# Performance work log

Measured on AMD Instinct MI355X. Metric: run time of the kernel, lower is better.

Reference implementation:

```python
import jax, jax.numpy as jnp
import numpy as np
from jax import lax

H = 32  # hidden_dim

def _lstm_layer(x_tbd, W_ih, W_hh, b_ih, b_hh):
    """x_tbd: [T, B, D]. Returns all hidden states [T, B, H]. PyTorch gate order i,f,g,o."""
    T, B, _ = x_tbd.shape
    # Precompute input contribution for all timesteps (one big GEMM)
    xW = jnp.einsum('tbd,gd->tbg', x_tbd, W_ih) + (b_ih + b_hh)  # [T, B, 4H]
    W_hh_T = W_hh.T  # [H, 4H]

    def step(carry, xw):
        h, c = carry
        gates = xw + h @ W_hh_T  # [B, 4H]
        i, f, g, o = jnp.split(gates, 4, axis=-1)
        i = jax.nn.sigmoid(i)
        f = jax.nn.sigmoid(f)
        g = jnp.tanh(g)
        o = jax.nn.sigmoid(o)
        c = f * c + i * g
        h = o * jnp.tanh(c)
        return (h, c), h

    h0 = jnp.zeros((B, H), x_tbd.dtype)
    (_, _), hs = lax.scan(step, (h0, h0), xW)
    return hs  # [T, B, H]


def setup_inputs() -> dict:
    key = jax.random.key(0)
    ks = jax.random.split(key, 12)
    s = 0.1  # keep gates out of saturation
    return {
        'x': jax.random.normal(ks[0], (4096, 512, 4), jnp.float32),
        'W_ih0': jax.random.normal(ks[1], (4 * H, 4), jnp.float32) * s,
        'W_hh0': jax.random.normal(ks[2], (4 * H, H), jnp.float32) * s,
        'b_ih0': jax.random.normal(ks[3], (4 * H,), jnp.float32) * s,
        'b_hh0': jax.random.normal(ks[4], (4 * H,), jnp.float32) * s,
        'W_ih1': jax.random.normal(ks[5], (4 * H, H), jnp.float32) * s,
        'W_hh1': jax.random.normal(ks[6], (4 * H, H), jnp.float32) * s,
        'b_ih1': jax.random.normal(ks[7], (4 * H,), jnp.float32) * s,
        'b_hh1': jax.random.normal(ks[8], (4 * H,), jnp.float32) * s,
        'W_out': jax.random.normal(ks[9], (1, H), jnp.float32) * s,
        'b_out': jax.random.normal(ks[10], (1,), jnp.float32) * s,
    }


def reference(x, W_ih0, W_hh0, b_ih0, b_hh0, W_ih1, W_hh1, b_ih1, b_hh1, W_out, b_out):
    # x: [B, T, D] (batch_first). Eval mode -> inter-layer dropout is identity.
    x_tbd = jnp.transpose(x, (1, 0, 2))  # [T, B, D]
    h1 = _lstm_layer(x_tbd, W_ih0, W_hh0, b_ih0, b_hh0)  # [T, B, H]
    h2 = _lstm_layer(h1, W_ih1, W_hh1, b_ih1, b_hh1)     # [T, B, H]
    last = h2[-1]  # [B, H] == out[:, -1, :]
    return last @ W_out.T + b_out  # [B, 1]
```

## Files before the change

### kernel.cpp

```cpp
#include <hip/hip_runtime.h>
#include <cmath>

constexpr int T   = 512;
constexpr int D   = 4;
constexpr int H   = 32;
constexpr int BT  = 16;
constexpr int BLK = 256;

constexpr float LOG2E     = 1.44269504088896340736f;
constexpr float NEG2LOG2E = -2.88539008177792681472f;

constexpr int XSTRIDE = 4104;
constexpr int HSTR = 40;

typedef short bf8 __attribute__((ext_vector_type(8)));
typedef float f4  __attribute__((ext_vector_type(4)));
typedef float f2  __attribute__((ext_vector_type(2)));

static __device__ __forceinline__ short bf16_rtn(float v) {
    unsigned u = __float_as_uint(v);
    u += 0x7FFFu + ((u >> 16) & 1u);
    return (short)(u >> 16);
}

__global__ __launch_bounds__(BLK, 1) void lstm_bf16p(
    const float* __restrict__ x,
    const float* __restrict__ W_ih0, const float* __restrict__ W_hh0,
    const float* __restrict__ b_ih0, const float* __restrict__ b_hh0,
    const float* __restrict__ W_ih1, const float* __restrict__ W_hh1,
    const float* __restrict__ b_ih1, const float* __restrict__ b_hh1,
    const float* __restrict__ W_out, const float* __restrict__ b_out,
    float* __restrict__ out)
{
    __shared__ __align__(16) short xbf[16 * XSTRIDE];
    __shared__ __align__(16) short h0b[2][16][HSTR];
    __shared__ __align__(16) short h1b[2][16][HSTR];
    __shared__ __align__(16) float h1f[16][36];

    const int tid   = threadIdx.x;
    const int w     = tid >> 6;
    const int lane  = tid & 63;
    const int q     = lane >> 4;
    const int nl    = lane & 15;
    const int layer = w >> 1;
    const int ug    = (w & 1) << 4;
    const int b0    = blockIdx.x * BT;

    for (int idx = tid; idx < 16 * T; idx += BLK) {
        const int col = idx & 15;
        const int t   = idx >> 4;
        float4 xv = *(const float4*)(x + ((size_t)(b0 + col) * T + t) * D);
        bf8 v = {0, 0, 0, 0, 0, 0, 0, 0};
        v[0] = bf16_rtn(xv.x); v[1] = bf16_rtn(xv.y);
        v[2] = bf16_rtn(xv.z); v[3] = bf16_rtn(xv.w);
        *(bf8*)&xbf[col * XSTRIDE + t * 8] = v;
    }
    for (int idx = tid; idx < 2 * 16 * HSTR; idx += BLK) {
        (&h0b[0][0][0])[idx] = 0;
        (&h1b[0][0][0])[idx] = 0;
    }

    const float* W1 = layer ? W_ih1 : W_hh0;
    bf8 w1[4], w2[4];
    f4  bias[4];
    #pragma unroll
    for (int g = 0; g < 4; ++g) {
        const float sc = (g == 2) ? NEG2LOG2E : -LOG2E;
        const int row = 32 * g + ug + nl;
        #pragma unroll
        for (int j = 0; j < 8; ++j) {
            w1[g][j] = bf16_rtn(W1[row * H + 8 * q + j] * sc);
            float v2 = layer ? W_hh1[row * H + 8 * q + j]
                             : ((q == 0 && j < 4) ? W_ih0[row * D + j] : 0.0f);
            w2[g][j] = bf16_rtn(v2 * sc);
        }
        #pragma unroll
        for (int r = 0; r < 4; ++r) {
            const int gr = 32 * g + ug + 4 * q + r;
            bias[g][r] = sc * (layer ? (b_ih1[gr] + b_hh1[gr])
                                     : (b_ih0[gr] + b_hh0[gr]));
        }
    }

    f2 cA; cA.x = 0.0f; cA.y = 0.0f;
    f2 cB; cB.x = 0.0f; cB.y = 0.0f;

    const short* xcol = &xbf[nl * XSTRIDE];

    __syncthreads();

    auto actpair = [&](f2& c2, float zi0, float zi1, float zf0, float zf1,
                       float zg0, float zg1, float zo0, float zo1,
                       unsigned& pkd, f2& hv) {
        f2 ei, ef, eg, eo, ec;
        ei.x = __builtin_amdgcn_exp2f(zi0); ei.y = __builtin_amdgcn_exp2f(zi1);
        ef.x = __builtin_amdgcn_exp2f(zf0); ef.y = __builtin_amdgcn_exp2f(zf1);
        eg.x = __builtin_amdgcn_exp2f(zg0); eg.y = __builtin_amdgcn_exp2f(zg1);
        eo.x = __builtin_amdgcn_exp2f(zo0); eo.y = __builtin_amdgcn_exp2f(zo1);
        f2 D1 = 1.0f + ef;
        f2 D2 = (1.0f + ei) * (1.0f + eg);
        f2 Dm = D1 * D2;
        float R = __builtin_amdgcn_rcpf(Dm.x * Dm.y);
        f2 rD; rD.x = R * Dm.y; rD.y = R * Dm.x;
        c2 = (c2 * D2 + (1.0f - eg) * D1) * rD;
        ec.x = __builtin_amdgcn_exp2f(c2.x * NEG2LOG2E);
        ec.y = __builtin_amdgcn_exp2f(c2.y * NEG2LOG2E);
        f2 Do = (1.0f + eo) * (1.0f + ec);
        float Ro = __builtin_amdgcn_rcpf(Do.x * Do.y);
        f2 ro; ro.x = Ro * Do.y; ro.y = Ro * Do.x;
        hv = (1.0f - ec) * ro;
        asm("v_cvt_pk_bf16_f32 %0, %1, %2" : "=v"(pkd) : "v"(hv.x), "v"(hv.y));
    };

    auto body = [&](const int i, const int rb, const int wb) {
        bf8 b2;
        if (layer == 0) {
            b2 = *(const bf8*)&xcol[(i & (T - 1)) * 8];
        } else {
            b2 = *(const bf8*)&h1b[rb][nl][8 * q];
        }
        bf8 b1 = *(const bf8*)&h0b[rb][nl][8 * q];

        f4 acc[4];
        #pragma unroll
        for (int g = 0; g < 4; ++g) {
            f4 A = __builtin_amdgcn_mfma_f32_16x16x32_bf16(w2[g], b2, bias[g], 0, 0, 0);
            A    = __builtin_amdgcn_mfma_f32_16x16x32_bf16(w1[g], b1, A,       0, 0, 0);
            acc[g] = A;
        }

        const bool act = layer ? (i >= 1) : (i < T);
        if (act) {
            unsigned pk0, pk1;
            f2 hvA, hvB;
            actpair(cA, acc[0][0], acc[0][1], acc[1][0], acc[1][1],
                        acc[2][0], acc[2][1], acc[3][0], acc[3][1], pk0, hvA);
            actpair(cB, acc[0][2], acc[0][3], acc[1][2], acc[1][3],
                        acc[2][2], acc[2][3], acc[3][2], acc[3][3], pk1, hvB);
            int2 hh; hh.x = (int)pk0; hh.y = (int)pk1;
            if (layer == 0) {
                *(int2*)&h0b[wb][nl][ug + 4 * q] = hh;
            } else {
                *(int2*)&h1b[wb][nl][ug + 4 * q] = hh;
                if (i == T) {
                    float4 hw;
                    hw.x = hvA.x; hw.y = hvA.y; hw.z = hvB.x; hw.w = hvB.y;
                    *(float4*)&h1f[nl][ug + 4 * q] = hw;
                }
            }
        }
        __syncthreads();
    };

    #pragma unroll 1
    for (int i = 0; i < T; i += 2) {
        body(i,     0, 1);
        body(i + 1, 1, 0);
    }
    body(T, 0, 1);

    if (tid < BT) {
        float acc = b_out[0];
        #pragma unroll
        for (int u = 0; u < H; ++u) acc = fmaf(W_out[u], h1f[tid][u], acc);
        out[b0 + tid] = acc;
    }
}

extern "C" void kernel_launch(void* const* d_in, const int* in_sizes, int n_in,
                              void* d_out, int out_size, void* d_ws, size_t ws_size,
                              hipStream_t stream) {
    const float* x     = (const float*)d_in[0];
    const float* W_ih0 = (const float*)d_in[1];
    const float* W_hh0 = (const float*)d_in[2];
    const float* b_ih0 = (const float*)d_in[3];
    const float* b_hh0 = (const float*)d_in[4];
    const float* W_ih1 = (const float*)d_in[5];
    const float* W_hh1 = (const float*)d_in[6];
    const float* b_ih1 = (const float*)d_in[7];
    const float* b_hh1 = (const float*)d_in[8];
    const float* W_out = (const float*)d_in[9];
    const float* b_out = (const float*)d_in[10];
    float* out = (float*)d_out;

    const int B = out_size;
    lstm_bf16p<<<B / BT, BLK, 0, stream>>>(x, W_ih0, W_hh0, b_ih0, b_hh0,
                                           W_ih1, W_hh1, b_ih1, b_hh1,
                                           W_out, b_out, out);
}
```

Measured before the change: 276.4 us.

## Replace per-step block barriers with LDS flag handshakes and 4-slot ring buffers

Swaps the __syncthreads after every timestep for per-wave progress flags in shared memory, with spin-waits using s_sleep. Hidden states move into 4-slot ring buffers so layer-0 waves can run up to three steps ahead of layer-1 waves. The aim is to stop the two layers and the four waves from advancing in lockstep, so they can overlap and barrier stalls drop. The cost is volatile LDS polling, extra fences, and sleep latency that may wake waves later than a hardware barrier would.

```diff
diff --git a/kernel.cpp b/kernel.cpp
--- a/kernel.cpp
+++ b/kernel.cpp
@@ -6,6 +6,7 @@
 constexpr int H   = 32;
 constexpr int BT  = 16;
 constexpr int BLK = 256;
+constexpr int NSL = 4;
 
 constexpr float LOG2E     = 1.44269504088896340736f;
 constexpr float NEG2LOG2E = -2.88539008177792681472f;
@@ -23,7 +24,7 @@
     return (short)(u >> 16);
 }
 
-__global__ __launch_bounds__(BLK, 1) void lstm_bf16p(
+__global__ __launch_bounds__(BLK, 1) void lstm_flag(
     const float* __restrict__ x,
     const float* __restrict__ W_ih0, const float* __restrict__ W_hh0,
     const float* __restrict__ b_ih0, const float* __restrict__ b_hh0,
@@ -33,9 +34,10 @@
     float* __restrict__ out)
 {
     __shared__ __align__(16) short xbf[16 * XSTRIDE];
-    __shared__ __align__(16) short h0b[2][16][HSTR];
-    __shared__ __align__(16) short h1b[2][16][HSTR];
+    __shared__ __align__(16) short h0r[NSL][16][HSTR];
+    __shared__ __align__(16) short h1r[NSL][16][HSTR];
     __shared__ __align__(16) float h1f[16][36];
+    __shared__ __align__(16) int   flg[4];
 
     const int tid   = threadIdx.x;
     const int w     = tid >> 6;
@@ -55,10 +57,11 @@
         v[2] = bf16_rtn(xv.z); v[3] = bf16_rtn(xv.w);
         *(bf8*)&xbf[col * XSTRIDE + t * 8] = v;
     }
-    for (int idx = tid; idx < 2 * 16 * HSTR; idx += BLK) {
-        (&h0b[0][0][0])[idx] = 0;
-        (&h1b[0][0][0])[idx] = 0;
-    }
+    for (int idx = tid; idx < NSL * 16 * HSTR; idx += BLK) {
+        (&h0r[0][0][0])[idx] = 0;
+        (&h1r[0][0][0])[idx] = 0;
+    }
+    if (tid < 4) flg[tid] = 0;
 
     const float* W1 = layer ? W_ih1 : W_hh0;
     bf8 w1[4], w2[4];
@@ -112,52 +115,66 @@
         asm("v_cvt_pk_bf16_f32 %0, %1, %2" : "=v"(pkd) : "v"(hv.x), "v"(hv.y));
     };
 
-    auto body = [&](const int i, const int rb, const int wb) {
-        bf8 b2;
-        if (layer == 0) {
-            b2 = *(const bf8*)&xcol[(i & (T - 1)) * 8];
-        } else {
-            b2 = *(const bf8*)&h1b[rb][nl][8 * q];
-        }
-        bf8 b1 = *(const bf8*)&h0b[rb][nl][8 * q];
-
-        f4 acc[4];
-        #pragma unroll
-        for (int g = 0; g < 4; ++g) {
-            f4 A = __builtin_amdgcn_mfma_f32_16x16x32_bf16(w2[g], b2, bias[g], 0, 0, 0);
-            A    = __builtin_amdgcn_mfma_f32_16x16x32_bf16(w1[g], b1, A,       0, 0, 0);
-            acc[g] = A;
-        }
-
-        const bool act = layer ? (i >= 1) : (i < T);
-        if (act) {
-            unsigned pk0, pk1;
-            f2 hvA, hvB;
+    volatile int* vf = flg;
+
+    if (layer == 0) {
+        #pragma unroll 1
+        for (int i = 0; i < T; ++i) {
+            while ((vf[w ^ 1] < i) | (vf[2] < i - 3) | (vf[3] < i - 3))
+                __builtin_amdgcn_s_sleep(1);
+            __threadfence_block();
+            bf8 b2 = *(const bf8*)&xcol[i * 8];
+            bf8 b1 = *(const bf8*)&h0r[(i - 1) & (NSL - 1)][nl][8 * q];
+            f4 acc[4];
+            #pragma unroll
+            for (int g = 0; g < 4; ++g) {
+                f4 A = __builtin_amdgcn_mfma_f32_16x16x32_bf16(w2[g], b2, bias[g], 0, 0, 0);
+                A    = __builtin_amdgcn_mfma_f32_16x16x32_bf16(w1[g], b1, A,       0, 0, 0);
+                acc[g] = A;
+            }
+            unsigned pk0, pk1; f2 hvA, hvB;
             actpair(cA, acc[0][0], acc[0][1], acc[1][0], acc[1][1],
                         acc[2][0], acc[2][1], acc[3][0], acc[3][1], pk0, hvA);
             actpair(cB, acc[0][2], acc[0][3], acc[1][2], acc[1][3],
                         acc[2][2], acc[2][3], acc[3][2], acc[3][3], pk1, hvB);
             int2 hh; hh.x = (int)pk0; hh.y = (int)pk1;
-            if (layer == 0) {
-                *(int2*)&h0b[wb][nl][ug + 4 * q] = hh;
-            } else {
-                *(int2*)&h1b[wb][nl][ug + 4 * q] = hh;
-                if (i == T) {
-                    float4 hw;
-                    hw.x = hvA.x; hw.y = hvA.y; hw.z = hvB.x; hw.w = hvB.y;
-                    *(float4*)&h1f[nl][ug + 4 * q] = hw;
-                }
+            *(int2*)&h0r[i & (NSL - 1)][nl][ug + 4 * q] = hh;
+            __threadfence_block();
+            vf[w] = i + 1;
+        }
+    } else {
+        #pragma unroll 1
+        for (int j = 0; j < T; ++j) {
+            while ((vf[w ^ 1] < j) | (vf[0] < j + 1) | (vf[1] < j + 1))
+                __builtin_amdgcn_s_sleep(1);
+            __threadfence_block();
+            bf8 b2 = *(const bf8*)&h1r[(j - 1) & (NSL - 1)][nl][8 * q];
+            bf8 b1 = *(const bf8*)&h0r[j & (NSL - 1)][nl][8 * q];
+            f4 acc[4];
+            #pragma unroll
+            for (int g = 0; g < 4; ++g) {
+                f4 A = __builtin_amdgcn_mfma_f32_16x16x32_bf16(w2[g], b2, bias[g], 0, 0, 0);
+                A    = __builtin_amdgcn_mfma_f32_16x16x32_bf16(w1[g], b1, A,       0, 0, 0);
+                acc[g] = A;
             }
-        }
-        __syncthreads();
-    };
-
-    #pragma unroll 1
-    for (int i = 0; i < T; i += 2) {
-        body(i,     0, 1);
-        body(i + 1, 1, 0);
-    }
-    body(T, 0, 1);
+            unsigned pk0, pk1; f2 hvA, hvB;
+            actpair(cA, acc[0][0], acc[0][1], acc[1][0], acc[1][1],
+                        acc[2][0], acc[2][1], acc[3][0], acc[3][1], pk0, hvA);
+            actpair(cB, acc[0][2], acc[0][3], acc[1][2], acc[1][3],
+                        acc[2][2], acc[2][3], acc[3][2], acc[3][3], pk1, hvB);
+            int2 hh; hh.x = (int)pk0; hh.y = (int)pk1;
+            *(int2*)&h1r[j & (NSL - 1)][nl][ug + 4 * q] = hh;
+            if (j == T - 1) {
+                float4 hw;
+                hw.x = hvA.x; hw.y = hvA.y; hw.z = hvB.x; hw.w = hvB.y;
+                *(float4*)&h1f[nl][ug + 4 * q] = hw;
+            }
+            __threadfence_block();
+            vf[w] = j + 1;
+        }
+    }
+
+    __syncthreads();
 
     if (tid < BT) {
         float acc = b_out[0];
@@ -184,7 +201,7 @@
     float* out = (float*)d_out;
 
     const int B = out_size;
-    lstm_bf16p<<<B / BT, BLK, 0, stream>>>(x, W_ih0, W_hh0, b_ih0, b_hh0,
-                                           W_ih1, W_hh1, b_ih1, b_hh1,
-                                           W_out, b_out, out);
+    lstm_flag<<<B / BT, BLK, 0, stream>>>(x, W_ih0, W_hh0, b_ih0, b_hh0,
+                                          W_ih1, W_hh1, b_ih1, b_hh1,
+                                          W_out, b_out, out);
 }
```

Result: slower. 362.0 us (+31.0%).
